# Performance work log

Hardware: AMD Instinct MI355X
Metric: run time of the kernel (lower is better)

The kernel has to match this reference:

```python
import jax, jax.numpy as jnp
import numpy as np

B, N_PER, D, L, DEG = 16, 2048, 128, 4, 16
N = B * N_PER
E = N * DEG
MSG_EPS = 1e-7  # GENConv message eps


def _lin_init(k, fi, fo):
    kw, kb = jax.random.split(k)
    s = 1.0 / np.sqrt(fi)
    W = jax.random.uniform(kw, (fi, fo), jnp.float32, minval=-s, maxval=s)
    b = jax.random.uniform(kb, (fo,), jnp.float32, minval=-s, maxval=s)
    return W, b


def setup_inputs() -> dict:
    key = jax.random.key(0)
    ks = jax.random.split(key, 6 + 2 * L)
    flat_c = jax.random.normal(ks[0], (N,), jnp.float32)
    edge_weight = jax.random.normal(ks[1], (E,), jnp.float32)
    # edges confined within each graph: local indices + per-graph offset
    e_per = N_PER * DEG
    local = jax.random.randint(ks[2], (2, B, e_per), 0, N_PER, jnp.int32)
    offs = (jnp.arange(B, dtype=jnp.int32) * N_PER)[None, :, None]
    edge_index = (local + offs).reshape(2, E)
    node_W, node_b = _lin_init(ks[3], 1, D)
    edge_W, edge_b = _lin_init(ks[4], 1, D)
    W1l, b1l, W2l, b2l = [], [], [], []
    for i in range(L):
        w1, bb1 = _lin_init(ks[6 + 2 * i], D, 2 * D)
        w2, bb2 = _lin_init(ks[7 + 2 * i], 2 * D, D)
        W1l.append(w1); b1l.append(bb1); W2l.append(w2); b2l.append(bb2)
    lin_W, lin_b = _lin_init(ks[5], D, 1)
    return dict(
        flat_c=flat_c, edge_weight=edge_weight, edge_index=edge_index,
        node_W=node_W, node_b=node_b, edge_W=edge_W, edge_b=edge_b,
        ts=jnp.ones((L,), jnp.float32),
        W1=jnp.stack(W1l), b1=jnp.stack(b1l),
        g1=jnp.ones((L, 2 * D), jnp.float32), be1=jnp.zeros((L, 2 * D), jnp.float32),
        W2=jnp.stack(W2l), b2=jnp.stack(b2l),
        ln_g=jnp.ones((L, D), jnp.float32), ln_b=jnp.zeros((L, D), jnp.float32),
        lin_W=lin_W, lin_b=lin_b)


def _layernorm(x, g, b, eps=1e-5):
    mu = jnp.mean(x, -1, keepdims=True)
    var = jnp.mean((x - mu) ** 2, -1, keepdims=True)
    return (x - mu) * jax.lax.rsqrt(var + eps) * g + b


def _gen_conv(x, edge_attr, src, dst, t, W1, b1, g1, be1, W2, b2):
    # GENConv with softmax aggregation (per-destination, per-channel)
    m = jax.nn.relu(x[src] + edge_attr) + MSG_EPS          # [E, D]
    logits = m * t
    mx = jax.ops.segment_max(logits, dst, num_segments=N)  # [N, D]
    ex = jnp.exp(logits - mx[dst])
    denom = jax.ops.segment_sum(ex, dst, num_segments=N)
    alpha = ex / (denom[dst] + 1e-16)
    aggr = jax.ops.segment_sum(m * alpha, dst, num_segments=N)  # [N, D]
    h = aggr + x
    # MLP: Linear(D,2D) -> LayerNorm -> ReLU -> Linear(2D,D)
    h = jax.nn.relu(_layernorm(h @ W1 + b1, g1, be1))
    return h @ W2 + b2


def reference(flat_c, edge_weight, edge_index, node_W, node_b, edge_W, edge_b,
              ts, W1, b1, g1, be1, W2, b2, ln_g, ln_b, lin_W, lin_b):
    src, dst = edge_index[0], edge_index[1]
    x = flat_c[:, None] @ node_W + node_b              # [N, D]
    ea = edge_weight[:, None] @ edge_W + edge_b        # [E, D]
    # first layer: raw conv only (pre-activation 'res+' scheme)
    x = _gen_conv(x, ea, src, dst, ts[0], W1[0], b1[0], g1[0], be1[0], W2[0], b2[0])
    for l in range(1, L):
        h = x
        z = jax.nn.relu(_layernorm(x, ln_g[l], ln_b[l]))  # dropout=identity (eval)
        x = _gen_conv(z, ea, src, dst, ts[l], W1[l], b1[l], g1[l], be1[l], W2[l], b2[l]) + h
    x = jax.nn.relu(_layernorm(x, ln_g[0], ln_b[0]))
    x = x @ lin_W + lin_b                              # [N, 1]
    out = x.reshape(B, N_PER)                          # equal-size graphs, max_len = N_PER
    return out - out[:, :1]                            # subtract first-node output per graph
```

## Files before the change

kernel.cpp:

```cpp
#include <hip/hip_runtime.h>
#include <hip/hip_bf16.h>
#include <stdint.h>

#define NN   32768
#define EE   524288
#define DD   128
#define D2   256
#define NPER 2048

using f32x4 = __attribute__((ext_vector_type(4))) float;
using sh8   = __attribute__((ext_vector_type(8))) short;
using sh4   = __attribute__((ext_vector_type(4))) short;

__device__ inline uint32_t rtn_hi_bits(float x){
  uint32_t u = __float_as_uint(x);
  return (u + 0x7FFFu + ((u >> 16) & 1u)) & 0xFFFF0000u;
}

__device__ inline int swz_node(int blk, int wave){
  int s = (blk & 7) * 1024 + (blk >> 3);
  return s * 4 + wave;
}

__global__ void k_count(const int* __restrict__ dst, int* __restrict__ cnt){
  int e = blockIdx.x * 256 + threadIdx.x;
  if (e < EE) atomicAdd(&cnt[dst[e]], 1);
}

__global__ __launch_bounds__(1024)
void k_scan(const int* __restrict__ cnt, int* __restrict__ rowptr){
  __shared__ int ps[1024];
  int t = threadIdx.x;
  int loc[32];
  int base = t * 32;
  int s = 0;
  #pragma unroll
  for (int j = 0; j < 32; ++j){ loc[j] = cnt[base + j]; s += loc[j]; }
  ps[t] = s; __syncthreads();
  for (int off = 1; off < 1024; off <<= 1){
    int v = (t >= off) ? ps[t - off] : 0;
    __syncthreads();
    ps[t] += v;
    __syncthreads();
  }
  int run = ps[t] - s;
  #pragma unroll
  for (int j = 0; j < 32; ++j){ rowptr[base + j] = run; run += loc[j]; }
  if (t == 1023) rowptr[NN] = run;
}

__global__ void k_scatter(const int* __restrict__ src, const int* __restrict__ dst,
                          const float* __restrict__ w, const int* __restrict__ rowptr,
                          int* __restrict__ cur, int* __restrict__ es, float* __restrict__ ew){
  int e = blockIdx.x * 256 + threadIdx.x;
  if (e < EE){
    int d = dst[e];
    int pos = rowptr[d] + atomicAdd(&cur[d], 1);
    es[pos] = src[e];
    ew[pos] = w[e];
  }
}

__global__ __launch_bounds__(256)
void k_packw(const float* __restrict__ W1, const float* __restrict__ W2,
             ushort* __restrict__ W1h, ushort* __restrict__ W1l,
             ushort* __restrict__ W2h, ushort* __restrict__ W2l){
  if (blockIdx.x < 64){
    int t = blockIdx.x * 256 + threadIdx.x;
    int lane = t & 63, mt = (t >> 6) & 15, kt = (t >> 10) & 3, layer = t >> 12;
    int nl = lane & 15, g = lane >> 4;
    int ucol = mt * 16 + nl;
    const float* Wp = W1 + layer * (DD * D2);
    sh8 hh, ll;
    #pragma unroll
    for (int j = 0; j < 8; ++j){
      int k = kt * 32 + g * 4 + (j & 3) + 16 * (j >> 2);
      float v = Wp[k * D2 + ucol];
      uint32_t hb = rtn_hi_bits(v);
      hh[j] = (short)(hb >> 16);
      ll[j] = (short)(__float_as_uint(v - __uint_as_float(hb)) >> 16);
    }
    *(sh8*)(W1h + t * 8) = hh;
    *(sh8*)(W1l + t * 8) = ll;
  } else {
    int t = (blockIdx.x - 64) * 256 + threadIdx.x;
    int lane = t & 63, mt = (t >> 6) & 7, kt = (t >> 9) & 7, layer = t >> 12;
    int nl = lane & 15, g = lane >> 4;
    int xcol = mt * 16 + nl;
    const float* Wp = W2 + layer * (D2 * DD);
    sh8 hh, ll;
    #pragma unroll
    for (int j = 0; j < 8; ++j){
      int k = kt * 32 + g * 4 + (j & 3) + 16 * (j >> 2);
      float v = Wp[k * DD + xcol];
      uint32_t hb = rtn_hi_bits(v);
      hh[j] = (short)(hb >> 16);
      ll[j] = (short)(__float_as_uint(v - __uint_as_float(hb)) >> 16);
    }
    *(sh8*)(W2h + t * 8) = hh;
    *(sh8*)(W2l + t * 8) = ll;
  }
}

template<int MODE>
__global__ __launch_bounds__(256)
void k_edge(const float* __restrict__ Zf, const float* __restrict__ cvec,
            const float* __restrict__ nW, const float* __restrict__ nb,
            const int* __restrict__ rowptr,
            const int* __restrict__ es, const float* __restrict__ ew,
            const float* __restrict__ eW, const float* __restrict__ eB,
            const float* __restrict__ ts, int layer,
            ushort* __restrict__ Hh, ushort* __restrict__ Hl){
  int n  = swz_node(blockIdx.x, threadIdx.x >> 6);
  int ld = threadIdx.x & 63;
  int d0 = ld * 2;
  float t  = ts[layer];
  float wx = eW[d0], wy = eW[d0 + 1];
  float bx = eB[d0], by = eB[d0 + 1];
  float nwx = 0.f, nwy = 0.f, nbx = 0.f, nby = 0.f;
  if (MODE == 0){ nwx = nW[d0]; nwy = nW[d0 + 1]; nbx = nb[d0]; nby = nb[d0 + 1]; }
  int r0 = __builtin_amdgcn_readfirstlane(rowptr[n]);
  int r1 = __builtin_amdgcn_readfirstlane(rowptr[n + 1]);

  float s0a = 0.f, s1a = 0.f, a0a = 0.f, a1a = 0.f;

  auto body = [&](float zx, float zy, float wj){
    float m0 = fmaxf(zx + fmaf(wj, wx, bx), 0.f) + 1e-7f;
    float m1 = fmaxf(zy + fmaf(wj, wy, by), 0.f) + 1e-7f;
    float p0 = __expf(fminf(m0 * t, 60.f));
    float p1 = __expf(fminf(m1 * t, 60.f));
    s0a += p0; a0a = fmaf(p0, m0, a0a);
    s1a += p1; a1a = fmaf(p1, m1, a1a);
  };

  int j = r0;
  for (; j + 4 <= r1; j += 4){
    int   sA = es[j],     sB = es[j + 1], sC = es[j + 2], sD = es[j + 3];
    float wA = ew[j],     wB = ew[j + 1], wC = ew[j + 2], wD = ew[j + 3];
    float zAx, zAy, zBx, zBy, zCx, zCy, zDx, zDy;
    if (MODE == 0){
      float cA = cvec[sA], cB = cvec[sB], cC = cvec[sC], cD = cvec[sD];
      zAx = fmaf(cA, nwx, nbx); zAy = fmaf(cA, nwy, nby);
      zBx = fmaf(cB, nwx, nbx); zBy = fmaf(cB, nwy, nby);
      zCx = fmaf(cC, nwx, nbx); zCy = fmaf(cC, nwy, nby);
      zDx = fmaf(cD, nwx, nbx); zDy = fmaf(cD, nwy, nby);
    } else {
      float2 zA = *(const float2*)(Zf + (size_t)sA * DD + d0);
      float2 zB = *(const float2*)(Zf + (size_t)sB * DD + d0);
      float2 zC = *(const float2*)(Zf + (size_t)sC * DD + d0);
      float2 zD = *(const float2*)(Zf + (size_t)sD * DD + d0);
      zAx = zA.x; zAy = zA.y; zBx = zB.x; zBy = zB.y;
      zCx = zC.x; zCy = zC.y; zDx = zD.x; zDy = zD.y;
    }
    body(zAx, zAy, wA); body(zBx, zBy, wB);
    body(zCx, zCy, wC); body(zDx, zDy, wD);
  }
  for (; j < r1; ++j){
    int s = es[j]; float w = ew[j];
    float zx, zy;
    if (MODE == 0){
      float cs = cvec[s];
      zx = fmaf(cs, nwx, nbx); zy = fmaf(cs, nwy, nby);
    } else {
      float2 z = *(const float2*)(Zf + (size_t)s * DD + d0);
      zx = z.x; zy = z.y;
    }
    body(zx, zy, w);
  }

  float znx, zny;
  if (MODE == 0){
    float cn = cvec[n];
    znx = fmaf(cn, nwx, nbx); zny = fmaf(cn, nwy, nby);
  } else {
    float2 zn2 = *(const float2*)(Zf + (size_t)n * DD + d0);
    znx = zn2.x; zny = zn2.y;
  }
  float hx = fmaf(a0a, __builtin_amdgcn_rcpf(s0a + 1e-16f), znx);
  float hy = fmaf(a1a, __builtin_amdgcn_rcpf(s1a + 1e-16f), zny);
  uint32_t hbx = rtn_hi_bits(hx), hby = rtn_hi_bits(hy);
  uint32_t hw = (hbx >> 16) | (hby & 0xFFFF0000u);
  float lx = hx - __uint_as_float(hbx), ly = hy - __uint_as_float(hby);
  uint32_t lw = (__float_as_uint(lx) >> 16) | (__float_as_uint(ly) & 0xFFFF0000u);
  ((uint32_t*)(Hh + (size_t)n * DD))[ld] = hw;
  ((uint32_t*)(Hl + (size_t)n * DD))[ld] = lw;
}

__global__ __launch_bounds__(256, 2)
void k_mlp(const ushort* __restrict__ Hhi, const ushort* __restrict__ Hlo,
           const ushort* __restrict__ W1h, const ushort* __restrict__ W1l,
           const float* __restrict__ b1, const float* __restrict__ g1,
           const float* __restrict__ be1,
           const ushort* __restrict__ W2h, const ushort* __restrict__ W2l,
           const float* __restrict__ b2, const float* __restrict__ Xres,
           float* __restrict__ Xout,
           const float* __restrict__ lnG, const float* __restrict__ lnB,
           float* __restrict__ Zout, int hasRes, int writeX)
{
  __shared__ ushort Ufh[16384];
  __shared__ ushort Ufl[16384];
  __shared__ float2 Pln[256];

  const int tid = threadIdx.x;
  const int w = tid >> 6, l = tid & 63, nl = l & 15, g = l >> 4;
  const int bs = (blockIdx.x & 7) * 64 + (blockIdx.x >> 3);
  const int n0 = bs * 64;

  f32x4 acc[4][4];
  #pragma unroll
  for (int mi = 0; mi < 4; ++mi)
    #pragma unroll
    for (int nt = 0; nt < 4; ++nt) acc[mi][nt] = (f32x4)0.f;

  const int hbase = (n0 + nl) * DD + g * 4;

  #pragma unroll
  for (int kt = 0; kt < 4; ++kt){
    sh8 ah[4], al[4];
    #pragma unroll
    for (int mi = 0; mi < 4; ++mi){
      int fi = ((kt * 16 + w * 4 + mi) * 64 + l) * 8;
      ah[mi] = *(const sh8*)(W1h + fi);
      al[mi] = *(const sh8*)(W1l + fi);
    }
    sh8 bh[4], bl[4];
    #pragma unroll
    for (int nt = 0; nt < 4; ++nt){
      int hi_ = hbase + nt * 16 * DD + kt * 32;
      sh8 vh, vl;
      ((sh4*)&vh)[0] = *(const sh4*)(Hhi + hi_);
      ((sh4*)&vh)[1] = *(const sh4*)(Hhi + hi_ + 16);
      ((sh4*)&vl)[0] = *(const sh4*)(Hlo + hi_);
      ((sh4*)&vl)[1] = *(const sh4*)(Hlo + hi_ + 16);
      bh[nt] = vh; bl[nt] = vl;
    }
    #pragma unroll
    for (int mi = 0; mi < 4; ++mi)
      #pragma unroll
      for (int nt = 0; nt < 4; ++nt){
        acc[mi][nt] = __builtin_amdgcn_mfma_f32_16x16x32_bf16(ah[mi], bh[nt], acc[mi][nt], 0, 0, 0);
        acc[mi][nt] = __builtin_amdgcn_mfma_f32_16x16x32_bf16(ah[mi], bl[nt], acc[mi][nt], 0, 0, 0);
        acc[mi][nt] = __builtin_amdgcn_mfma_f32_16x16x32_bf16(al[mi], bh[nt], acc[mi][nt], 0, 0, 0);
      }
  }

  #pragma unroll
  for (int mi = 0; mi < 4; ++mi){
    f32x4 bv = *(const f32x4*)(b1 + w * 64 + mi * 16 + g * 4);
    #pragma unroll
    for (int nt = 0; nt < 4; ++nt) acc[mi][nt] += bv;
  }
  float s1[4], s2[4];
  #pragma unroll
  for (int nt = 0; nt < 4; ++nt){
    float a = 0.f, b = 0.f;
    #pragma unroll
    for (int mi = 0; mi < 4; ++mi)
      #pragma unroll
      for (int r = 0; r < 4; ++r){ float v = acc[mi][nt][r]; a += v; b += v * v; }
    a += __shfl_xor(a, 16); b += __shfl_xor(b, 16);
    a += __shfl_xor(a, 32); b += __shfl_xor(b, 32);
    s1[nt] = a; s2[nt] = b;
  }
  {
    float p1 = (g == 0) ? s1[0] : (g == 1) ? s1[1] : (g == 2) ? s1[2] : s1[3];
    float p2 = (g == 0) ? s2[0] : (g == 1) ? s2[1] : (g == 2) ? s2[2] : s2[3];
    Pln[(g * 16 + nl) * 4 + w] = make_float2(p1, p2);
  }
  __syncthreads();

  {
    f32x4 gv[4], ev[4];
    #pragma unroll
    for (int mi = 0; mi < 4; ++mi){
      gv[mi] = *(const f32x4*)(g1  + w * 64 + mi * 16 + g * 4);
      ev[mi] = *(const f32x4*)(be1 + w * 64 + mi * 16 + g * 4);
    }
    #pragma unroll
    for (int nt = 0; nt < 4; ++nt){
      int node = nt * 16 + nl;
      float t1 = 0.f, t2 = 0.f;
      #pragma unroll
      for (int wi = 0; wi < 4; ++wi){
        float2 pp = Pln[node * 4 + wi];
        t1 += pp.x; t2 += pp.y;
      }
      float mean = t1 * (1.f / D2);
      float var  = t2 * (1.f / D2) - mean * mean;
      float rstd = 1.f / sqrtf(var + 1e-5f);
      #pragma unroll
      for (int p = 0; p < 2; ++p){
        sh8 uh, ul;
        #pragma unroll
        for (int j = 0; j < 8; ++j){
          int mi = 2 * p + (j >> 2), r = j & 3;
          float v = (acc[mi][nt][r] - mean) * rstd * gv[mi][r] + ev[mi][r];
          v = fmaxf(v, 0.f);
          uint32_t hb = rtn_hi_bits(v);
          uh[j] = (short)(hb >> 16);
          ul[j] = (short)(__float_as_uint(v - __uint_as_float(hb)) >> 16);
        }
        int fo = (((2 * w + p) * 4 + nt) * 64 + l) * 8;
        *(sh8*)(Ufh + fo) = uh;
        *(sh8*)(Ufl + fo) = ul;
      }
    }
  }
  __syncthreads();

  f32x4 a2[2][4];
  #pragma unroll
  for (int mi = 0; mi < 2; ++mi)
    #pragma unroll
    for (int nt = 0; nt < 4; ++nt) a2[mi][nt] = (f32x4)0.f;
  #pragma unroll
  for (int kt = 0; kt < 8; ++kt){
    sh8 wh[2], wl[2];
    #pragma unroll
    for (int mi = 0; mi < 2; ++mi){
      int fi = ((kt * 8 + w * 2 + mi) * 64 + l) * 8;
      wh[mi] = *(const sh8*)(W2h + fi);
      wl[mi] = *(const sh8*)(W2l + fi);
    }
    sh8 uh[4], ul[4];
    #pragma unroll
    for (int nt = 0; nt < 4; ++nt){
      int fo = ((kt * 4 + nt) * 64 + l) * 8;
      uh[nt] = *(const sh8*)(Ufh + fo);
      ul[nt] = *(const sh8*)(Ufl + fo);
    }
    #pragma unroll
    for (int mi = 0; mi < 2; ++mi)
      #pragma unroll
      for (int nt = 0; nt < 4; ++nt){
        a2[mi][nt] = __builtin_amdgcn_mfma_f32_16x16x32_bf16(wh[mi], uh[nt], a2[mi][nt], 0, 0, 0);
        a2[mi][nt] = __builtin_amdgcn_mfma_f32_16x16x32_bf16(wh[mi], ul[nt], a2[mi][nt], 0, 0, 0);
        a2[mi][nt] = __builtin_amdgcn_mfma_f32_16x16x32_bf16(wl[mi], uh[nt], a2[mi][nt], 0, 0, 0);
      }
  }
  __syncthreads();

  float* Xb = (float*)Ufh;
  #pragma unroll
  for (int mi = 0; mi < 2; ++mi)
    #pragma unroll
    for (int nt = 0; nt < 4; ++nt){
      int node = nt * 16 + nl;
      int xc = (w * 2 + mi) * 16 + g * 4;
      int idx = node * DD + (xc ^ ((node & 7) << 2));
      *(f32x4*)(Xb + idx) = a2[mi][nt];
    }
  __syncthreads();

  {
    int en = tid >> 2, ec = tid & 3;
    f32x4 vr[8];
    float s1e = 0.f, s2e = 0.f;
    #pragma unroll
    for (int i = 0; i < 8; ++i){
      int q = ec + i * 4;
      int c = q * 4;
      int idx = en * DD + ((q ^ (en & 7)) << 2);
      f32x4 v = *(const f32x4*)(Xb + idx);
      v += *(const f32x4*)(b2 + c);
      if (hasRes) v += *(const f32x4*)(Xres + (size_t)(n0 + en) * DD + c);
      vr[i] = v;
      #pragma unroll
      for (int r = 0; r < 4; ++r){ s1e += v[r]; s2e += v[r] * v[r]; }
    }
    s1e += __shfl_xor(s1e, 1); s2e += __shfl_xor(s2e, 1);
    s1e += __shfl_xor(s1e, 2); s2e += __shfl_xor(s2e, 2);
    float mean = s1e * (1.f / DD);
    float var  = s2e * (1.f / DD) - mean * mean;
    float rs   = 1.f / sqrtf(var + 1e-5f);
    #pragma unroll
    for (int i = 0; i < 8; ++i){
      int q = ec + i * 4;
      int c = q * 4;
      if (writeX) *(f32x4*)(Xout + (size_t)(n0 + en) * DD + c) = vr[i];
      f32x4 gv = *(const f32x4*)(lnG + c);
      f32x4 bv = *(const f32x4*)(lnB + c);
      f32x4 z;
      #pragma unroll
      for (int r = 0; r < 4; ++r)
        z[r] = fmaxf((vr[i][r] - mean) * rs * gv[r] + bv[r], 0.f);
      *(f32x4*)(Zout + (size_t)(n0 + en) * DD + c) = z;
    }
  }
}

__global__ __launch_bounds__(256)
void k_fin(const float* __restrict__ Zf, const float* __restrict__ linW,
           float* __restrict__ out){
  int n  = swz_node(blockIdx.x, threadIdx.x >> 6);
  int d0 = (threadIdx.x & 63) * 2;
  int nb_ = n & ~(NPER - 1);
  float2 v  = *(const float2*)(Zf + (size_t)n  * DD + d0);
  float2 vb = *(const float2*)(Zf + (size_t)nb_ * DD + d0);
  float2 lw = *(const float2*)(linW + d0);
  float p = (v.x - vb.x) * lw.x + (v.y - vb.y) * lw.y;
  #pragma unroll
  for (int m = 1; m < 64; m <<= 1) p += __shfl_xor(p, m);
  if ((threadIdx.x & 63) == 0) out[n] = p;
}

extern "C" void kernel_launch(void* const* d_in, const int* in_sizes, int n_in,
                              void* d_out, int out_size, void* d_ws, size_t ws_size,
                              hipStream_t stream){
  const float* flat_c = (const float*)d_in[0];
  const float* edge_w = (const float*)d_in[1];
  const int*   eidx   = (const int*)  d_in[2];
  const float* nodeW  = (const float*)d_in[3];
  const float* nodeB  = (const float*)d_in[4];
  const float* edgeW  = (const float*)d_in[5];
  const float* edgeB  = (const float*)d_in[6];
  const float* ts     = (const float*)d_in[7];
  const float* W1     = (const float*)d_in[8];
  const float* b1     = (const float*)d_in[9];
  const float* g1     = (const float*)d_in[10];
  const float* be1    = (const float*)d_in[11];
  const float* W2     = (const float*)d_in[12];
  const float* b2     = (const float*)d_in[13];
  const float* lng    = (const float*)d_in[14];
  const float* lnb    = (const float*)d_in[15];
  const float* linW   = (const float*)d_in[16];
  float* out = (float*)d_out;

  char* wsp = (char*)d_ws;
  size_t off = 0;
  auto alloc = [&](size_t bytes) -> void* {
    void* p = wsp + off;
    off += (bytes + 255) & ~(size_t)255;
    return p;
  };
  float*  bufA = (float*) alloc((size_t)NN * DD * 4);
  float*  bufB = (float*) alloc((size_t)NN * DD * 4);
  ushort* Hhi  = (ushort*)alloc((size_t)NN * DD * 2);
  ushort* Hlo  = (ushort*)alloc((size_t)NN * DD * 2);
  ushort* W1h  = (ushort*)alloc((size_t)4 * 32768 * 2);
  ushort* W1l  = (ushort*)alloc((size_t)4 * 32768 * 2);
  ushort* W2h  = (ushort*)alloc((size_t)4 * 32768 * 2);
  ushort* W2l  = (ushort*)alloc((size_t)4 * 32768 * 2);
  int*   cnt   = (int*)  alloc((size_t)NN * 4);
  int*   cur   = (int*)  alloc((size_t)NN * 4);
  int*   rowpt = (int*)  alloc((size_t)(NN + 1) * 4);
  int*   es    = (int*)  alloc((size_t)EE * 4);
  float* ewS   = (float*)alloc((size_t)EE * 4);
  if (off > ws_size) return;

  const int* srcI = eidx;
  const int* dstI = eidx + EE;

  (void)hipMemsetAsync(cnt, 0, (size_t)2 * NN * 4, stream);
  k_count  <<<EE / 256, 256, 0, stream>>>(dstI, cnt);
  k_scan   <<<1, 1024, 0, stream>>>(cnt, rowpt);
  k_scatter<<<EE / 256, 256, 0, stream>>>(srcI, dstI, edge_w, rowpt, cur, es, ewS);
  k_packw  <<<128, 256, 0, stream>>>(W1, W2, W1h, W1l, W2h, W2l);

  for (int l = 0; l < 4; ++l){
    if (l == 0)
      k_edge<0><<<NN / 4, 256, 0, stream>>>(nullptr, flat_c, nodeW, nodeB,
                                            rowpt, es, ewS, edgeW, edgeB, ts, l, Hhi, Hlo);
    else
      k_edge<1><<<NN / 4, 256, 0, stream>>>(bufA, nullptr, nullptr, nullptr,
                                            rowpt, es, ewS, edgeW, edgeB, ts, l, Hhi, Hlo);
    int nx = (l + 1) & 3;
    k_mlp <<<NN / 64, 256, 0, stream>>>(Hhi, Hlo,
                                        W1h + (size_t)l * 32768, W1l + (size_t)l * 32768,
                                        b1 + l * D2, g1 + l * D2, be1 + l * D2,
                                        W2h + (size_t)l * 32768, W2l + (size_t)l * 32768,
                                        b2 + l * DD, bufB, bufB,
                                        lng + nx * DD, lnb + nx * DD, bufA,
                                        l > 0 ? 1 : 0, l < 3 ? 1 : 0);
  }
  k_fin<<<NN / 4, 256, 0, stream>>>(bufA, linW, out);
}
```

Measured before the change: 308.6 us.

## Process two nodes per wave in edge kernel, halve MLP LDS, fuse count and pack

The edge-aggregation kernel now handles two adjacent destination nodes per wave, interleaving their masked 4-edge gather batches so more independent loads are in flight. The MLP kernel keeps the intermediate bf16 hi/lo tiles in registers and stages them into a single half-sized shared buffer in two K-stages, which allows launch bounds of 3 blocks per CU instead of 2. The edge-count and weight-pack kernels are merged into one launch. In exchange, the edge kernel does masked redundant loads on uneven degrees, the MLP kernel adds extra barriers, and the higher occupancy target may force register spills.

```diff
diff --git a/kernel.cpp b/kernel.cpp
--- a/kernel.cpp
+++ b/kernel.cpp
@@ -15,16 +15,6 @@
 __device__ inline uint32_t rtn_hi_bits(float x){
   uint32_t u = __float_as_uint(x);
   return (u + 0x7FFFu + ((u >> 16) & 1u)) & 0xFFFF0000u;
-}
-
-__device__ inline int swz_node(int blk, int wave){
-  int s = (blk & 7) * 1024 + (blk >> 3);
-  return s * 4 + wave;
-}
-
-__global__ void k_count(const int* __restrict__ dst, int* __restrict__ cnt){
-  int e = blockIdx.x * 256 + threadIdx.x;
-  if (e < EE) atomicAdd(&cnt[dst[e]], 1);
 }
 
 __global__ __launch_bounds__(1024)
@@ -62,11 +52,16 @@
 }
 
 __global__ __launch_bounds__(256)
-void k_packw(const float* __restrict__ W1, const float* __restrict__ W2,
-             ushort* __restrict__ W1h, ushort* __restrict__ W1l,
-             ushort* __restrict__ W2h, ushort* __restrict__ W2l){
-  if (blockIdx.x < 64){
-    int t = blockIdx.x * 256 + threadIdx.x;
+void k_count_pack(const int* __restrict__ dst, int* __restrict__ cnt,
+                  const float* __restrict__ W1, const float* __restrict__ W2,
+                  ushort* __restrict__ W1h, ushort* __restrict__ W1l,
+                  ushort* __restrict__ W2h, ushort* __restrict__ W2l){
+  int b = blockIdx.x;
+  if (b < 2048){
+    int e = b * 256 + threadIdx.x;
+    atomicAdd(&cnt[dst[e]], 1);
+  } else if (b < 2112){
+    int t = (b - 2048) * 256 + threadIdx.x;
     int lane = t & 63, mt = (t >> 6) & 15, kt = (t >> 10) & 3, layer = t >> 12;
     int nl = lane & 15, g = lane >> 4;
     int ucol = mt * 16 + nl;
@@ -83,7 +78,7 @@
     *(sh8*)(W1h + t * 8) = hh;
     *(sh8*)(W1l + t * 8) = ll;
   } else {
-    int t = (blockIdx.x - 64) * 256 + threadIdx.x;
+    int t = (b - 2112) * 256 + threadIdx.x;
     int lane = t & 63, mt = (t >> 6) & 7, kt = (t >> 9) & 7, layer = t >> 12;
     int nl = lane & 15, g = lane >> 4;
     int xcol = mt * 16 + nl;
@@ -111,7 +106,10 @@
             const float* __restrict__ eW, const float* __restrict__ eB,
             const float* __restrict__ ts, int layer,
             ushort* __restrict__ Hh, ushort* __restrict__ Hl){
-  int n  = swz_node(blockIdx.x, threadIdx.x >> 6);
+  int wv = threadIdx.x >> 6;
+  int s8 = (blockIdx.x & 7) * 512 + (blockIdx.x >> 3);
+  int nA = s8 * 8 + wv * 2;
+  int nB = nA + 1;
   int ld = threadIdx.x & 63;
   int d0 = ld * 2;
   float t  = ts[layer];
@@ -119,74 +117,104 @@
   float bx = eB[d0], by = eB[d0 + 1];
   float nwx = 0.f, nwy = 0.f, nbx = 0.f, nby = 0.f;
   if (MODE == 0){ nwx = nW[d0]; nwy = nW[d0 + 1]; nbx = nb[d0]; nby = nb[d0 + 1]; }
-  int r0 = __builtin_amdgcn_readfirstlane(rowptr[n]);
-  int r1 = __builtin_amdgcn_readfirstlane(rowptr[n + 1]);
-
-  float s0a = 0.f, s1a = 0.f, a0a = 0.f, a1a = 0.f;
-
-  auto body = [&](float zx, float zy, float wj){
-    float m0 = fmaxf(zx + fmaf(wj, wx, bx), 0.f) + 1e-7f;
-    float m1 = fmaxf(zy + fmaf(wj, wy, by), 0.f) + 1e-7f;
-    float p0 = __expf(fminf(m0 * t, 60.f));
-    float p1 = __expf(fminf(m1 * t, 60.f));
-    s0a += p0; a0a = fmaf(p0, m0, a0a);
-    s1a += p1; a1a = fmaf(p1, m1, a1a);
-  };
-
-  int j = r0;
-  for (; j + 4 <= r1; j += 4){
-    int   sA = es[j],     sB = es[j + 1], sC = es[j + 2], sD = es[j + 3];
-    float wA = ew[j],     wB = ew[j + 1], wC = ew[j + 2], wD = ew[j + 3];
-    float zAx, zAy, zBx, zBy, zCx, zCy, zDx, zDy;
+  int r0A = __builtin_amdgcn_readfirstlane(rowptr[nA]);
+  int r1A = __builtin_amdgcn_readfirstlane(rowptr[nB]);
+  int r1B = __builtin_amdgcn_readfirstlane(rowptr[nB + 1]);
+  int jA = r0A, jB = r1A;
+
+  float sA0 = 0.f, sA1 = 0.f, aA0 = 0.f, aA1 = 0.f;
+  float sB0 = 0.f, sB1 = 0.f, aB0 = 0.f, aB1 = 0.f;
+
+  int dA = r1A - r0A, dB = r1B - r1A;
+  int iters = ((dA > dB ? dA : dB) + 3) >> 2;
+
+  for (int it = 0; it < iters; ++it){
+    float zxA[4], zyA[4], wvA[4], mkA[4];
+    float zxB[4], zyB[4], wvB[4], mkB[4];
+    bool doA = jA < r1A, doB = jB < r1B;
+    if (doA){
+      #pragma unroll
+      for (int u = 0; u < 4; ++u){
+        int j = jA + u;
+        int je = j < r1A ? j : r1A - 1;
+        mkA[u] = j < r1A ? 1.f : 0.f;
+        int si = es[je]; wvA[u] = ew[je];
+        if (MODE == 0){
+          float cs = cvec[si];
+          zxA[u] = fmaf(cs, nwx, nbx); zyA[u] = fmaf(cs, nwy, nby);
+        } else {
+          float2 z = *(const float2*)(Zf + (size_t)si * DD + d0);
+          zxA[u] = z.x; zyA[u] = z.y;
+        }
+      }
+    }
+    if (doB){
+      #pragma unroll
+      for (int u = 0; u < 4; ++u){
+        int j = jB + u;
+        int je = j < r1B ? j : r1B - 1;
+        mkB[u] = j < r1B ? 1.f : 0.f;
+        int si = es[je]; wvB[u] = ew[je];
+        if (MODE == 0){
+          float cs = cvec[si];
+          zxB[u] = fmaf(cs, nwx, nbx); zyB[u] = fmaf(cs, nwy, nby);
+        } else {
+          float2 z = *(const float2*)(Zf + (size_t)si * DD + d0);
+          zxB[u] = z.x; zyB[u] = z.y;
+        }
+      }
+    }
+    if (doA){
+      #pragma unroll
+      for (int u = 0; u < 4; ++u){
+        float m0 = fmaxf(zxA[u] + fmaf(wvA[u], wx, bx), 0.f) + 1e-7f;
+        float m1 = fmaxf(zyA[u] + fmaf(wvA[u], wy, by), 0.f) + 1e-7f;
+        float p0 = __expf(fminf(m0 * t, 60.f)) * mkA[u];
+        float p1 = __expf(fminf(m1 * t, 60.f)) * mkA[u];
+        sA0 += p0; aA0 = fmaf(p0, m0, aA0);
+        sA1 += p1; aA1 = fmaf(p1, m1, aA1);
+      }
+      jA += 4;
+    }
+    if (doB){
+      #pragma unroll
+      for (int u = 0; u < 4; ++u){
+        float m0 = fmaxf(zxB[u] + fmaf(wvB[u], wx, bx), 0.f) + 1e-7f;
+        float m1 = fmaxf(zyB[u] + fmaf(wvB[u], wy, by), 0.f) + 1e-7f;
+        float p0 = __expf(fminf(m0 * t, 60.f)) * mkB[u];
+        float p1 = __expf(fminf(m1 * t, 60.f)) * mkB[u];
+        sB0 += p0; aB0 = fmaf(p0, m0, aB0);
+        sB1 += p1; aB1 = fmaf(p1, m1, aB1);
+      }
+      jB += 4;
+    }
+  }
+
+  #pragma unroll
+  for (int q = 0; q < 2; ++q){
+    int   n  = q ? nB : nA;
+    float s0 = q ? sB0 : sA0, s1 = q ? sB1 : sA1;
+    float a0 = q ? aB0 : aA0, a1 = q ? aB1 : aA1;
+    float znx, zny;
     if (MODE == 0){
-      float cA = cvec[sA], cB = cvec[sB], cC = cvec[sC], cD = cvec[sD];
-      zAx = fmaf(cA, nwx, nbx); zAy = fmaf(cA, nwy, nby);
-      zBx = fmaf(cB, nwx, nbx); zBy = fmaf(cB, nwy, nby);
-      zCx = fmaf(cC, nwx, nbx); zCy = fmaf(cC, nwy, nby);
-      zDx = fmaf(cD, nwx, nbx); zDy = fmaf(cD, nwy, nby);
+      float cn = cvec[n];
+      znx = fmaf(cn, nwx, nbx); zny = fmaf(cn, nwy, nby);
     } else {
-      float2 zA = *(const float2*)(Zf + (size_t)sA * DD + d0);
-      float2 zB = *(const float2*)(Zf + (size_t)sB * DD + d0);
-      float2 zC = *(const float2*)(Zf + (size_t)sC * DD + d0);
-      float2 zD = *(const float2*)(Zf + (size_t)sD * DD + d0);
-      zAx = zA.x; zAy = zA.y; zBx = zB.x; zBy = zB.y;
-      zCx = zC.x; zCy = zC.y; zDx = zD.x; zDy = zD.y;
-    }
-    body(zAx, zAy, wA); body(zBx, zBy, wB);
-    body(zCx, zCy, wC); body(zDx, zDy, wD);
-  }
-  for (; j < r1; ++j){
-    int s = es[j]; float w = ew[j];
-    float zx, zy;
-    if (MODE == 0){
-      float cs = cvec[s];
-      zx = fmaf(cs, nwx, nbx); zy = fmaf(cs, nwy, nby);
-    } else {
-      float2 z = *(const float2*)(Zf + (size_t)s * DD + d0);
-      zx = z.x; zy = z.y;
-    }
-    body(zx, zy, w);
-  }
-
-  float znx, zny;
-  if (MODE == 0){
-    float cn = cvec[n];
-    znx = fmaf(cn, nwx, nbx); zny = fmaf(cn, nwy, nby);
-  } else {
-    float2 zn2 = *(const float2*)(Zf + (size_t)n * DD + d0);
-    znx = zn2.x; zny = zn2.y;
-  }
-  float hx = fmaf(a0a, __builtin_amdgcn_rcpf(s0a + 1e-16f), znx);
-  float hy = fmaf(a1a, __builtin_amdgcn_rcpf(s1a + 1e-16f), zny);
-  uint32_t hbx = rtn_hi_bits(hx), hby = rtn_hi_bits(hy);
-  uint32_t hw = (hbx >> 16) | (hby & 0xFFFF0000u);
-  float lx = hx - __uint_as_float(hbx), ly = hy - __uint_as_float(hby);
-  uint32_t lw = (__float_as_uint(lx) >> 16) | (__float_as_uint(ly) & 0xFFFF0000u);
-  ((uint32_t*)(Hh + (size_t)n * DD))[ld] = hw;
-  ((uint32_t*)(Hl + (size_t)n * DD))[ld] = lw;
-}
-
-__global__ __launch_bounds__(256, 2)
+      float2 zn2 = *(const float2*)(Zf + (size_t)n * DD + d0);
+      znx = zn2.x; zny = zn2.y;
+    }
+    float hx = fmaf(a0, __builtin_amdgcn_rcpf(s0 + 1e-16f), znx);
+    float hy = fmaf(a1, __builtin_amdgcn_rcpf(s1 + 1e-16f), zny);
+    uint32_t hbx = rtn_hi_bits(hx), hby = rtn_hi_bits(hy);
+    uint32_t hw = (hbx >> 16) | (hby & 0xFFFF0000u);
+    float lx = hx - __uint_as_float(hbx), ly = hy - __uint_as_float(hby);
+    uint32_t lw = (__float_as_uint(lx) >> 16) | (__float_as_uint(ly) & 0xFFFF0000u);
+    ((uint32_t*)(Hh + (size_t)n * DD))[ld] = hw;
+    ((uint32_t*)(Hl + (size_t)n * DD))[ld] = lw;
+  }
+}
+
+__global__ __launch_bounds__(256, 3)
 void k_mlp(const ushort* __restrict__ Hhi, const ushort* __restrict__ Hlo,
            const ushort* __restrict__ W1h, const ushort* __restrict__ W1l,
            const float* __restrict__ b1, const float* __restrict__ g1,
@@ -197,8 +225,7 @@
            const float* __restrict__ lnG, const float* __restrict__ lnB,
            float* __restrict__ Zout, int hasRes, int writeX)
 {
-  __shared__ ushort Ufh[16384];
-  __shared__ ushort Ufl[16384];
+  __shared__ ushort Ubuf[16384];
   __shared__ float2 Pln[256];
 
   const int tid = threadIdx.x;
@@ -269,6 +296,7 @@
   }
   __syncthreads();
 
+  sh8 fh[2][4], fl[2][4];
   {
     f32x4 gv[4], ev[4];
     #pragma unroll
@@ -300,47 +328,65 @@
           uh[j] = (short)(hb >> 16);
           ul[j] = (short)(__float_as_uint(v - __uint_as_float(hb)) >> 16);
         }
-        int fo = (((2 * w + p) * 4 + nt) * 64 + l) * 8;
-        *(sh8*)(Ufh + fo) = uh;
-        *(sh8*)(Ufl + fo) = ul;
-      }
+        fh[p][nt] = uh; fl[p][nt] = ul;
+      }
+    }
+  }
+
+  ushort* Ufh = Ubuf;
+  ushort* Ufl = Ubuf + 8192;
+  f32x4 a2[2][4];
+  #pragma unroll
+  for (int mi = 0; mi < 2; ++mi)
+    #pragma unroll
+    for (int nt = 0; nt < 4; ++nt) a2[mi][nt] = (f32x4)0.f;
+
+  #pragma unroll
+  for (int stage = 0; stage < 2; ++stage){
+    __syncthreads();
+    if ((w >> 1) == stage){
+      int wl_ = w & 1;
+      #pragma unroll
+      for (int p = 0; p < 2; ++p)
+        #pragma unroll
+        for (int nt = 0; nt < 4; ++nt){
+          int ktL = 2 * wl_ + p;
+          int fo = ((ktL * 4 + nt) * 64 + l) * 8;
+          *(sh8*)(Ufh + fo) = fh[p][nt];
+          *(sh8*)(Ufl + fo) = fl[p][nt];
+        }
+    }
+    __syncthreads();
+    #pragma unroll
+    for (int ktL = 0; ktL < 4; ++ktL){
+      int kt = stage * 4 + ktL;
+      sh8 wh[2], wl2[2];
+      #pragma unroll
+      for (int mi = 0; mi < 2; ++mi){
+        int fi = ((kt * 8 + w * 2 + mi) * 64 + l) * 8;
+        wh[mi]  = *(const sh8*)(W2h + fi);
+        wl2[mi] = *(const sh8*)(W2l + fi);
+      }
+      sh8 uh[4], ul[4];
+      #pragma unroll
+      for (int nt = 0; nt < 4; ++nt){
+        int fo = ((ktL * 4 + nt) * 64 + l) * 8;
+        uh[nt] = *(const sh8*)(Ufh + fo);
+        ul[nt] = *(const sh8*)(Ufl + fo);
+      }
+      #pragma unroll
+      for (int mi = 0; mi < 2; ++mi)
+        #pragma unroll
+        for (int nt = 0; nt < 4; ++nt){
+          a2[mi][nt] = __builtin_amdgcn_mfma_f32_16x16x32_bf16(wh[mi],  uh[nt], a2[mi][nt], 0, 0, 0);
+          a2[mi][nt] = __builtin_amdgcn_mfma_f32_16x16x32_bf16(wh[mi],  ul[nt], a2[mi][nt], 0, 0, 0);
+          a2[mi][nt] = __builtin_amdgcn_mfma_f32_16x16x32_bf16(wl2[mi], uh[nt], a2[mi][nt], 0, 0, 0);
+        }
     }
   }
   __syncthreads();
 
-  f32x4 a2[2][4];
-  #pragma unroll
-  for (int mi = 0; mi < 2; ++mi)
-    #pragma unroll
-    for (int nt = 0; nt < 4; ++nt) a2[mi][nt] = (f32x4)0.f;
-  #pragma unroll
-  for (int kt = 0; kt < 8; ++kt){
-    sh8 wh[2], wl[2];
-    #pragma unroll
-    for (int mi = 0; mi < 2; ++mi){
-      int fi = ((kt * 8 + w * 2 + mi) * 64 + l) * 8;
-      wh[mi] = *(const sh8*)(W2h + fi);
-      wl[mi] = *(const sh8*)(W2l + fi);
-    }
-    sh8 uh[4], ul[4];
-    #pragma unroll
-    for (int nt = 0; nt < 4; ++nt){
-      int fo = ((kt * 4 + nt) * 64 + l) * 8;
-      uh[nt] = *(const sh8*)(Ufh + fo);
-      ul[nt] = *(const sh8*)(Ufl + fo);
-    }
-    #pragma unroll
-    for (int mi = 0; mi < 2; ++mi)
-      #pragma unroll
-      for (int nt = 0; nt < 4; ++nt){
-        a2[mi][nt] = __builtin_amdgcn_mfma_f32_16x16x32_bf16(wh[mi], uh[nt], a2[mi][nt], 0, 0, 0);
-        a2[mi][nt] = __builtin_amdgcn_mfma_f32_16x16x32_bf16(wh[mi], ul[nt], a2[mi][nt], 0, 0, 0);
-        a2[mi][nt] = __builtin_amdgcn_mfma_f32_16x16x32_bf16(wl[mi], uh[nt], a2[mi][nt], 0, 0, 0);
-      }
-  }
-  __syncthreads();
-
-  float* Xb = (float*)Ufh;
+  float* Xb = (float*)Ubuf;
   #pragma unroll
   for (int mi = 0; mi < 2; ++mi)
     #pragma unroll
@@ -392,7 +438,8 @@
 __global__ __launch_bounds__(256)
 void k_fin(const float* __restrict__ Zf, const float* __restrict__ linW,
            float* __restrict__ out){
-  int n  = swz_node(blockIdx.x, threadIdx.x >> 6);
+  int blk = blockIdx.x;
+  int n = ((blk & 7) * 1024 + (blk >> 3)) * 4 + (threadIdx.x >> 6);
   int d0 = (threadIdx.x & 63) * 2;
   int nb_ = n & ~(NPER - 1);
   float2 v  = *(const float2*)(Zf + (size_t)n  * DD + d0);
@@ -452,17 +499,16 @@
   const int* dstI = eidx + EE;
 
   (void)hipMemsetAsync(cnt, 0, (size_t)2 * NN * 4, stream);
-  k_count  <<<EE / 256, 256, 0, stream>>>(dstI, cnt);
+  k_count_pack<<<2176, 256, 0, stream>>>(dstI, cnt, W1, W2, W1h, W1l, W2h, W2l);
   k_scan   <<<1, 1024, 0, stream>>>(cnt, rowpt);
   k_scatter<<<EE / 256, 256, 0, stream>>>(srcI, dstI, edge_w, rowpt, cur, es, ewS);
-  k_packw  <<<128, 256, 0, stream>>>(W1, W2, W1h, W1l, W2h, W2l);
 
   for (int l = 0; l < 4; ++l){
     if (l == 0)
-      k_edge<0><<<NN / 4, 256, 0, stream>>>(nullptr, flat_c, nodeW, nodeB,
+      k_edge<0><<<NN / 8, 256, 0, stream>>>(nullptr, flat_c, nodeW, nodeB,
                                             rowpt, es, ewS, edgeW, edgeB, ts, l, Hhi, Hlo);
     else
-      k_edge<1><<<NN / 4, 256, 0, stream>>>(bufA, nullptr, nullptr, nullptr,
+      k_edge<1><<<NN / 8, 256, 0, stream>>>(bufA, nullptr, nullptr, nullptr,
                                             rowpt, es, ewS, edgeW, edgeB, ts, l, Hhi, Hlo);
     int nx = (l + 1) & 3;
     k_mlp <<<NN / 64, 256, 0, stream>>>(Hhi, Hlo,
```

New measurement: 338.9 us. +9.8%, slower.
